# Kernel optimization log

Hardware: AMD Instinct MI355X
Metric: run time of the kernel (lower is better)

Reference implementation:

```python
import jax, jax.numpy as jnp
import numpy as np

B, S, HID = 1, 8192, 768
H, D = 12, 64          # num heads, head dim (HID = H*D)
W = 256                # one-sided attention window


def _shift_chunks(xc, C):
    # xc: [B, C, w, H, D] -> prev/next chunk copies padded with zeros
    prev = jnp.pad(xc, ((0, 0), (1, 0), (0, 0), (0, 0), (0, 0)))[:, :C]
    nxt = jnp.pad(xc, ((0, 0), (0, 1), (0, 0), (0, 0), (0, 0)))[:, 1:]
    return jnp.concatenate([prev, xc, nxt], axis=2)  # [B, C, 3w, H, D]


def sliding_window_attention(q, k, v, w):
    # q,k,v: [B, S, H, D]; q already scaled. Band width 2w+1.
    b, s, h, d = q.shape
    c = s // w
    qc = q.reshape(b, c, w, h, d)
    k3 = _shift_chunks(k.reshape(b, c, w, h, d), c)  # [b,c,3w,h,d]
    v3 = _shift_chunks(v.reshape(b, c, w, h, d), c)
    # scores of each query chunk against its 3-chunk key neighborhood
    scores3 = jnp.einsum('bcxhd,bcyhd->bhcxy', qc, k3)  # [b,h,c,w,3w]
    rows = jnp.arange(w)
    offs = jnp.arange(2 * w + 1)
    gidx = rows[:, None] + offs[None, :]  # [w, 2w+1] local key index p+j
    band = scores3[..., rows[:, None], gidx]  # [b,h,c,w,2w+1]
    # mask keys outside [0, S) (same effect as mask_invalid_locations)
    gq = jnp.arange(s).reshape(c, w)                    # global query pos
    keypos = gq[..., None] + (offs - w)                 # [c,w,2w+1]
    valid = (keypos >= 0) & (keypos < s)
    band = jnp.where(valid[None, None], band, -jnp.inf)
    prob = jax.nn.softmax(band, axis=-1)
    prob = jnp.where(valid[None, None], prob, 0.0)
    # scatter band probs back to 3w layout, then banded PV matmul
    prob3 = jnp.zeros(band.shape[:-1] + (3 * w,), band.dtype)
    prob3 = prob3.at[..., rows[:, None], gidx].set(prob)  # [b,h,c,w,3w]
    ctx = jnp.einsum('bhcxy,bcyhd->bcxhd', prob3, v3)
    return ctx.reshape(b, s, h, d)


def setup_inputs() -> dict:
    key = jax.random.key(0)
    ks = jax.random.split(key, 4)
    sc = 1.0 / np.sqrt(HID)
    return {
        'hidden_states': jax.random.normal(ks[0], (B, S, HID), jnp.float32),
        'Wq': jax.random.normal(ks[1], (HID, HID), jnp.float32) * sc,
        'bq': jnp.zeros((HID,), jnp.float32),
        'Wk': jax.random.normal(ks[2], (HID, HID), jnp.float32) * sc,
        'bk': jnp.zeros((HID,), jnp.float32),
        'Wv': jax.random.normal(ks[3], (HID, HID), jnp.float32) * sc,
        'bv': jnp.zeros((HID,), jnp.float32),
    }


def reference(hidden_states, Wq, bq, Wk, bk, Wv, bv):
    b, s, hid = hidden_states.shape
    q = (hidden_states @ Wq + bq).reshape(b, s, H, D)
    k = (hidden_states @ Wk + bk).reshape(b, s, H, D)
    v = (hidden_states @ Wv + bv).reshape(b, s, H, D)
    q = q / jnp.asarray(np.sqrt(D), q.dtype)
    ctx = sliding_window_attention(q, k, v, W)  # [b,s,H,D]
    return ctx.reshape(b, s, hid)
```

## Files before the change

kernel.cpp:

```cpp
#include <hip/hip_runtime.h>
#include <hip/hip_bf16.h>

#define S_LEN 8192
#define HID 768
#define NH 12
#define HD 64
#define WIN 256

typedef __bf16 bf16x8 __attribute__((ext_vector_type(8)));
typedef float f32x4 __attribute__((ext_vector_type(4)));
using bf16_t = __hip_bfloat16;

#define MFMA(a, b, c) __builtin_amdgcn_mfma_f32_16x16x32_bf16(a, b, c, 0, 0, 0)

__device__ __forceinline__ void gl2lds16(const bf16_t* g, bf16_t* l) {
  __builtin_amdgcn_global_load_lds(
      (const __attribute__((address_space(1))) void*)g,
      (__attribute__((address_space(3))) void*)l, 16, 0, 0);
}

__global__ __launch_bounds__(256) void prep(const float* __restrict__ hs,
                                            bf16_t* __restrict__ hb,
                                            const float* __restrict__ Wq,
                                            const float* __restrict__ Wk,
                                            const float* __restrict__ Wv,
                                            bf16_t* __restrict__ Wt) {
  int bx = blockIdx.x;
  int tid = threadIdx.x;
  if (bx < 6144) {
    int i = (bx * 256 + tid) * 4;
    float4 v = *reinterpret_cast<const float4*>(hs + i);
    union { ushort4 u; bf16_t b[4]; } H;
    H.b[0] = __float2bfloat16(v.x);
    H.b[1] = __float2bfloat16(v.y);
    H.b[2] = __float2bfloat16(v.z);
    H.b[3] = __float2bfloat16(v.w);
    *reinterpret_cast<ushort4*>(hb + i) = H.u;
    return;
  }
  __shared__ float t[32][33];
  int b = bx - 6144;
  int z = b / 576;
  int r = b % 576;
  int n0 = (r / 24) * 32, k0 = (r % 24) * 32;
  const float* src = (z == 0) ? Wq : ((z == 1) ? Wk : Wv);
  int tx = tid & 31, ty = tid >> 5;
  for (int i = 0; i < 4; ++i)
    t[ty + i * 8][tx] = src[(k0 + ty + i * 8) * HID + n0 + tx];
  __syncthreads();
  bf16_t* dst = Wt + z * HID * HID;
  for (int i = 0; i < 4; ++i)
    dst[(n0 + ty + i * 8) * HID + k0 + tx] = __float2bfloat16(t[tx][ty + i * 8]);
}

__global__ __launch_bounds__(256) void qkv_gemm(
    const bf16_t* __restrict__ hb, const bf16_t* __restrict__ Wt,
    const float* __restrict__ bq, const float* __restrict__ bk,
    const float* __restrict__ bv,
    bf16_t* __restrict__ Qw, bf16_t* __restrict__ Kw, bf16_t* __restrict__ Vt) {
  __shared__ __align__(16) bf16_t sA[2][128 * 64];
  __shared__ __align__(16) bf16_t sB[2][128 * 64];
  int m0 = blockIdx.x * 128;
  int zq = blockIdx.y / 6;
  int nn0 = (blockIdx.y % 6) * 128;
  int n0g = zq * HID + nn0;
  int tid = threadIdx.x;
  int w = tid >> 6, lane = tid & 63, lm = lane & 15, qd = lane >> 4;
  int wm = w & 1, wn = w >> 1;

  int srow = w * 8 + (lane >> 3);
  int sc8 = (lane & 7) ^ ((lane >> 3) & 7);
  const bf16_t* gA = hb + (m0 + srow) * HID + sc8 * 8;
  const bf16_t* gB = Wt + (n0g + srow) * HID + sc8 * 8;
  int sx0 = lm & 7;

#define QSTAGE(kk, bb)                                                     \
  {                                                                        \
    _Pragma("unroll") for (int u = 0; u < 4; ++u) {                        \
      gl2lds16(gA + (u * 32) * HID + (kk), sA[bb] + u * 2048 + w * 512);   \
      gl2lds16(gB + (u * 32) * HID + (kk), sB[bb] + u * 2048 + w * 512);   \
    }                                                                      \
  }

  QSTAGE(0, 0);
  __syncthreads();

  f32x4 acc[4][4] = {};
  for (int kt = 0; kt < 12; ++kt) {
    int b = kt & 1;
    if (kt < 11) QSTAGE((kt + 1) * 64, b ^ 1);
#pragma unroll
    for (int half = 0; half < 2; ++half) {
      int ca = (qd + 4 * half) ^ sx0;
      bf16x8 fa[4], fb[4];
#pragma unroll
      for (int i = 0; i < 4; ++i) {
        fa[i] = *reinterpret_cast<const bf16x8*>(
            sA[b] + (wm * 64 + i * 16 + lm) * 64 + ca * 8);
        fb[i] = *reinterpret_cast<const bf16x8*>(
            sB[b] + (wn * 64 + i * 16 + lm) * 64 + ca * 8);
      }
      if (zq == 2) {
#pragma unroll
        for (int i = 0; i < 4; ++i)
#pragma unroll
          for (int j = 0; j < 4; ++j)
            acc[i][j] = MFMA(fb[i], fa[j], acc[i][j]);
      } else {
#pragma unroll
        for (int i = 0; i < 4; ++i)
#pragma unroll
          for (int j = 0; j < 4; ++j)
            acc[i][j] = MFMA(fa[i], fb[j], acc[i][j]);
      }
    }
    __syncthreads();
  }

  if (zq != 2) {
    const float* bias = zq ? bk : bq;
    bf16_t* dst = zq ? Kw : Qw;
    float scale = zq ? 1.0f : 0.125f;
#pragma unroll
    for (int j = 0; j < 4; ++j) {
      int nl = nn0 + wn * 64 + j * 16 + lm;
      float bb = bias[nl];
      int h = nl >> 6, d = nl & 63;
#pragma unroll
      for (int i = 0; i < 4; ++i)
#pragma unroll
        for (int r = 0; r < 4; ++r) {
          int m = m0 + wm * 64 + i * 16 + qd * 4 + r;
          dst[(h * S_LEN + m) * HD + d] =
              __float2bfloat16((acc[i][j][r] + bb) * scale);
        }
    }
  } else {
#pragma unroll
    for (int i = 0; i < 4; ++i)
#pragma unroll
      for (int r = 0; r < 4; ++r) {
        int nl = nn0 + wn * 64 + i * 16 + qd * 4 + r;
        float bb = bv[nl];
#pragma unroll
        for (int j = 0; j < 4; ++j) {
          int m = m0 + wm * 64 + j * 16 + lm;
          Vt[nl * S_LEN + m] = __float2bfloat16(acc[i][j][r] + bb);
        }
      }
  }
}

__global__ __launch_bounds__(256, 4) void swa_kernel(
    const bf16_t* __restrict__ Qw, const bf16_t* __restrict__ Kw,
    const bf16_t* __restrict__ Vt, float* __restrict__ out) {
  __shared__ __align__(16) bf16_t sK[2][64 * 64];
  __shared__ __align__(16) bf16_t sV[2][64 * 64];
  __shared__ __align__(16) bf16_t sP[4 * 16 * 64];
  int h = blockIdx.y;
  int nb = blockIdx.x;
  int q0 = (((nb & 7) << 4) | (nb >> 3)) * 64;
  int tid = threadIdx.x;
  int w = tid >> 6, lane = tid & 63, lm = lane & 15, qd = lane >> 4;
  int xb = q0 + w * 16;

  int qoff = (h * S_LEN + xb + lm) * HD + qd * 8;
  bf16x8 aq0 = *reinterpret_cast<const bf16x8*>(Qw + qoff);
  bf16x8 aq1 = *reinterpret_cast<const bf16x8*>(Qw + qoff + 32);

  f32x4 o[4] = {};
  float lsum = 0.f;

  int y_begin = q0 - WIN; if (y_begin < 0) y_begin = 0;
  int y_end = q0 + 64 + WIN; if (y_end > S_LEN) y_end = S_LEN;
  int ntiles = (y_end - y_begin) >> 6;
  const bf16_t* Kh = Kw + h * S_LEN * HD;
  const bf16_t* Vh = Vt + h * HD * S_LEN;
  bf16_t* sPw = sP + w * 16 * 64;

  int srow = w * 8 + (lane >> 3);
  int sc8 = (lane & 7) ^ ((lane >> 3) & 7);
  int sx0 = lm & 7;

#define STAGE(y0, b)                                                    \
  {                                                                     \
    const bf16_t* kg = Kh + ((y0) + srow) * HD + sc8 * 8;               \
    gl2lds16(kg, &sK[b][w * 512]);                                      \
    gl2lds16(kg + 32 * HD, &sK[b][2048 + w * 512]);                     \
    const bf16_t* vg = Vh + srow * S_LEN + (y0) + sc8 * 8;              \
    gl2lds16(vg, &sV[b][w * 512]);                                      \
    gl2lds16(vg + 32 * S_LEN, &sV[b][2048 + w * 512]);                  \
  }

  STAGE(y_begin, 0);
  __syncthreads();

  for (int t = 0; t < ntiles; ++t) {
    int y0 = y_begin + t * 64;
    if (t + 1 < ntiles) STAGE(y0 + 64, (t + 1) & 1);
    int b = t & 1;
    f32x4 s[4] = {};
#pragma unroll
    for (int nt = 0; nt < 4; ++nt) {
      const bf16_t* kr = &sK[b][(nt * 16 + lm) * 64];
      bf16x8 b0 = *reinterpret_cast<const bf16x8*>(kr + (qd ^ sx0) * 8);
      bf16x8 b1 = *reinterpret_cast<const bf16x8*>(kr + ((qd + 4) ^ sx0) * 8);
      s[nt] = MFMA(b0, aq0, s[nt]);
      s[nt] = MFMA(b1, aq1, s[nt]);
    }
    int dy = y0 - q0;
    bool edge = (dy > 192) || (dy < -192);
#pragma unroll
    for (int nt = 0; nt < 4; ++nt) {
      union { ushort4 u; bf16_t b[4]; } P;
#pragma unroll
      for (int r = 0; r < 4; ++r) {
        float pv;
        if (edge) {
          int dlt = (y0 + nt * 16 + qd * 4 + r) - (xb + lm);
          pv = (dlt <= WIN && dlt >= -WIN) ? __expf(s[nt][r]) : 0.f;
        } else {
          pv = __expf(s[nt][r]);
        }
        lsum += pv;
        P.b[r] = __float2bfloat16(pv);
      }
      *reinterpret_cast<ushort4*>(
          sPw + lm * 64 + (((2 * nt + (qd >> 1)) ^ sx0) * 8) + (qd & 1) * 4) =
          P.u;
    }
    bf16x8 ap0 =
        *reinterpret_cast<const bf16x8*>(sPw + lm * 64 + ((qd ^ sx0) * 8));
    bf16x8 ap1 = *reinterpret_cast<const bf16x8*>(sPw + lm * 64 +
                                                  (((qd + 4) ^ sx0) * 8));
#pragma unroll
    for (int nt = 0; nt < 4; ++nt) {
      const bf16_t* vr = &sV[b][(nt * 16 + lm) * 64];
      bf16x8 v0 = *reinterpret_cast<const bf16x8*>(vr + (qd ^ sx0) * 8);
      bf16x8 v1 = *reinterpret_cast<const bf16x8*>(vr + ((qd + 4) ^ sx0) * 8);
      o[nt] = MFMA(ap0, v0, o[nt]);
      o[nt] = MFMA(ap1, v1, o[nt]);
    }
    __syncthreads();
  }
  lsum += __shfl_xor(lsum, 16);
  lsum += __shfl_xor(lsum, 32);
#pragma unroll
  for (int r = 0; r < 4; ++r) {
    float inv = 1.f / __shfl(lsum, qd * 4 + r);
    int x = xb + qd * 4 + r;
#pragma unroll
    for (int nt = 0; nt < 4; ++nt)
      out[x * HID + h * HD + nt * 16 + lm] = o[nt][r] * inv;
  }
}

extern "C" void kernel_launch(void* const* d_in, const int* in_sizes, int n_in,
                              void* d_out, int out_size, void* d_ws, size_t ws_size,
                              hipStream_t stream) {
  const float* hs = (const float*)d_in[0];
  const float* Wq = (const float*)d_in[1];
  const float* bq = (const float*)d_in[2];
  const float* Wk = (const float*)d_in[3];
  const float* bk = (const float*)d_in[4];
  const float* Wv = (const float*)d_in[5];
  const float* bv = (const float*)d_in[6];
  float* out = (float*)d_out;

  const int NSH = S_LEN * HID;
  const int NW = 3 * HID * HID;
  bf16_t* p = (bf16_t*)d_ws;
  bf16_t* hb = p; p += NSH;
  bf16_t* Wt = p; p += NW;
  bf16_t* Qw = p; p += NSH;
  bf16_t* Kw = p; p += NSH;
  bf16_t* Vt = p; p += NSH;

  prep<<<dim3(6144 + 1728), dim3(256), 0, stream>>>(hs, hb, Wq, Wk, Wv, Wt);
  qkv_gemm<<<dim3(64, 18), dim3(256), 0, stream>>>(
      hb, Wt, bq, bk, bv, Qw, Kw, Vt);
  swa_kernel<<<dim3(128, 12), dim3(256), 0, stream>>>(Qw, Kw, Vt, out);
}
```

Before: 161.3 us.

## Process 128 queries per block so each K/V tile serves two query groups

Each sliding-window attention block now covers 128 query rows instead of 64, with each wave handling two 16-row query groups against the same staged K/V tile. The aim is to amortize K/V global-to-LDS staging and LDS fragment reads over twice the queries, cutting redundant halo loads. In exchange the grid halves to 768 blocks, register and LDS use per block grow (launch bound lowered to 3 blocks), and each block iterates over more key tiles, some of them only partly inside the band for a given wave.

```diff
diff --git a/kernel.cpp b/kernel.cpp
--- a/kernel.cpp
+++ b/kernel.cpp
@@ -151,32 +151,34 @@
   }
 }
 
-__global__ __launch_bounds__(256, 4) void swa_kernel(
+__global__ __launch_bounds__(256, 3) void swa_kernel(
     const bf16_t* __restrict__ Qw, const bf16_t* __restrict__ Kw,
     const bf16_t* __restrict__ Vt, float* __restrict__ out) {
   __shared__ __align__(16) bf16_t sK[2][64 * 64];
   __shared__ __align__(16) bf16_t sV[2][64 * 64];
-  __shared__ __align__(16) bf16_t sP[4 * 16 * 64];
+  __shared__ __align__(16) bf16_t sP[4 * 32 * 64];
   int h = blockIdx.y;
   int nb = blockIdx.x;
-  int q0 = (((nb & 7) << 4) | (nb >> 3)) * 64;
+  int q0 = (((nb & 7) << 3) | (nb >> 3)) * 128;
   int tid = threadIdx.x;
   int w = tid >> 6, lane = tid & 63, lm = lane & 15, qd = lane >> 4;
-  int xb = q0 + w * 16;
+  int xb = q0 + w * 32;
 
   int qoff = (h * S_LEN + xb + lm) * HD + qd * 8;
-  bf16x8 aq0 = *reinterpret_cast<const bf16x8*>(Qw + qoff);
-  bf16x8 aq1 = *reinterpret_cast<const bf16x8*>(Qw + qoff + 32);
-
-  f32x4 o[4] = {};
-  float lsum = 0.f;
+  bf16x8 aq00 = *reinterpret_cast<const bf16x8*>(Qw + qoff);
+  bf16x8 aq01 = *reinterpret_cast<const bf16x8*>(Qw + qoff + 32);
+  bf16x8 aq10 = *reinterpret_cast<const bf16x8*>(Qw + qoff + 16 * HD);
+  bf16x8 aq11 = *reinterpret_cast<const bf16x8*>(Qw + qoff + 16 * HD + 32);
+
+  f32x4 o0[4] = {}, o1[4] = {};
+  float lsum0 = 0.f, lsum1 = 0.f;
 
   int y_begin = q0 - WIN; if (y_begin < 0) y_begin = 0;
-  int y_end = q0 + 64 + WIN; if (y_end > S_LEN) y_end = S_LEN;
+  int y_end = q0 + 128 + WIN; if (y_end > S_LEN) y_end = S_LEN;
   int ntiles = (y_end - y_begin) >> 6;
   const bf16_t* Kh = Kw + h * S_LEN * HD;
   const bf16_t* Vh = Vt + h * HD * S_LEN;
-  bf16_t* sPw = sP + w * 16 * 64;
+  bf16_t* sPw = sP + w * 32 * 64;
 
   int srow = w * 8 + (lane >> 3);
   int sc8 = (lane & 7) ^ ((lane >> 3) & 7);
@@ -199,59 +201,80 @@
     int y0 = y_begin + t * 64;
     if (t + 1 < ntiles) STAGE(y0 + 64, (t + 1) & 1);
     int b = t & 1;
-    f32x4 s[4] = {};
+    f32x4 s0[4] = {}, s1[4] = {};
 #pragma unroll
     for (int nt = 0; nt < 4; ++nt) {
       const bf16_t* kr = &sK[b][(nt * 16 + lm) * 64];
       bf16x8 b0 = *reinterpret_cast<const bf16x8*>(kr + (qd ^ sx0) * 8);
       bf16x8 b1 = *reinterpret_cast<const bf16x8*>(kr + ((qd + 4) ^ sx0) * 8);
-      s[nt] = MFMA(b0, aq0, s[nt]);
-      s[nt] = MFMA(b1, aq1, s[nt]);
-    }
-    int dy = y0 - q0;
-    bool edge = (dy > 192) || (dy < -192);
-#pragma unroll
-    for (int nt = 0; nt < 4; ++nt) {
-      union { ushort4 u; bf16_t b[4]; } P;
-#pragma unroll
-      for (int r = 0; r < 4; ++r) {
-        float pv;
-        if (edge) {
-          int dlt = (y0 + nt * 16 + qd * 4 + r) - (xb + lm);
-          pv = (dlt <= WIN && dlt >= -WIN) ? __expf(s[nt][r]) : 0.f;
-        } else {
-          pv = __expf(s[nt][r]);
+      s0[nt] = MFMA(b0, aq00, s0[nt]);
+      s0[nt] = MFMA(b1, aq01, s0[nt]);
+      s1[nt] = MFMA(b0, aq10, s1[nt]);
+      s1[nt] = MFMA(b1, aq11, s1[nt]);
+    }
+    int dyw = y0 - xb;
+    bool edge = (dyw > 193) || (dyw < -225);
+#pragma unroll
+    for (int g = 0; g < 2; ++g) {
+      const f32x4* sg = g ? s1 : s0;
+      float lacc = 0.f;
+#pragma unroll
+      for (int nt = 0; nt < 4; ++nt) {
+        union { ushort4 u; bf16_t b[4]; } P;
+#pragma unroll
+        for (int r = 0; r < 4; ++r) {
+          float pv;
+          if (edge) {
+            int dlt = (y0 + nt * 16 + qd * 4 + r) - (xb + g * 16 + lm);
+            pv = (dlt <= WIN && dlt >= -WIN) ? __expf(sg[nt][r]) : 0.f;
+          } else {
+            pv = __expf(sg[nt][r]);
+          }
+          lacc += pv;
+          P.b[r] = __float2bfloat16(pv);
         }
-        lsum += pv;
-        P.b[r] = __float2bfloat16(pv);
+        *reinterpret_cast<ushort4*>(
+            sPw + (g * 16 + lm) * 64 +
+            (((2 * nt + (qd >> 1)) ^ sx0) * 8) + (qd & 1) * 4) = P.u;
       }
-      *reinterpret_cast<ushort4*>(
-          sPw + lm * 64 + (((2 * nt + (qd >> 1)) ^ sx0) * 8) + (qd & 1) * 4) =
-          P.u;
-    }
-    bf16x8 ap0 =
+      if (g) lsum1 += lacc; else lsum0 += lacc;
+    }
+    bf16x8 ap00 =
         *reinterpret_cast<const bf16x8*>(sPw + lm * 64 + ((qd ^ sx0) * 8));
-    bf16x8 ap1 = *reinterpret_cast<const bf16x8*>(sPw + lm * 64 +
-                                                  (((qd + 4) ^ sx0) * 8));
+    bf16x8 ap01 = *reinterpret_cast<const bf16x8*>(sPw + lm * 64 +
+                                                   (((qd + 4) ^ sx0) * 8));
+    bf16x8 ap10 = *reinterpret_cast<const bf16x8*>(sPw + (16 + lm) * 64 +
+                                                   ((qd ^ sx0) * 8));
+    bf16x8 ap11 = *reinterpret_cast<const bf16x8*>(sPw + (16 + lm) * 64 +
+                                                   (((qd + 4) ^ sx0) * 8));
 #pragma unroll
     for (int nt = 0; nt < 4; ++nt) {
       const bf16_t* vr = &sV[b][(nt * 16 + lm) * 64];
       bf16x8 v0 = *reinterpret_cast<const bf16x8*>(vr + (qd ^ sx0) * 8);
       bf16x8 v1 = *reinterpret_cast<const bf16x8*>(vr + ((qd + 4) ^ sx0) * 8);
-      o[nt] = MFMA(ap0, v0, o[nt]);
-      o[nt] = MFMA(ap1, v1, o[nt]);
+      o0[nt] = MFMA(ap00, v0, o0[nt]);
+      o0[nt] = MFMA(ap01, v1, o0[nt]);
+      o1[nt] = MFMA(ap10, v0, o1[nt]);
+      o1[nt] = MFMA(ap11, v1, o1[nt]);
     }
     __syncthreads();
   }
-  lsum += __shfl_xor(lsum, 16);
-  lsum += __shfl_xor(lsum, 32);
+  lsum0 += __shfl_xor(lsum0, 16);
+  lsum0 += __shfl_xor(lsum0, 32);
+  lsum1 += __shfl_xor(lsum1, 16);
+  lsum1 += __shfl_xor(lsum1, 32);
 #pragma unroll
   for (int r = 0; r < 4; ++r) {
-    float inv = 1.f / __shfl(lsum, qd * 4 + r);
-    int x = xb + qd * 4 + r;
+    float inv0 = 1.f / __shfl(lsum0, qd * 4 + r);
+    int x0 = xb + qd * 4 + r;
 #pragma unroll
     for (int nt = 0; nt < 4; ++nt)
-      out[x * HID + h * HD + nt * 16 + lm] = o[nt][r] * inv;
+      out[x0 * HID + h * HD + nt * 16 + lm] = o0[nt][r] * inv0;
+    float inv1 = 1.f / __shfl(lsum1, qd * 4 + r);
+    int x1 = xb + 16 + qd * 4 + r;
+#pragma unroll
+    for (int nt = 0; nt < 4; ++nt)
+      out[x1 * HID + h * HD + nt * 16 + lm] = o1[nt][r] * inv1;
   }
 }
 
@@ -279,5 +302,5 @@
   prep<<<dim3(6144 + 1728), dim3(256), 0, stream>>>(hs, hb, Wq, Wk, Wv, Wt);
   qkv_gemm<<<dim3(64, 18), dim3(256), 0, stream>>>(
       hb, Wt, bq, bk, bv, Qw, Kw, Vt);
-  swa_kernel<<<dim3(128, 12), dim3(256), 0, stream>>>(Qw, Kw, Vt, out);
-}
+  swa_kernel<<<dim3(64, 12), dim3(256), 0, stream>>>(Qw, Kw, Vt, out);
+}
```

After: 160.1 us. Within noise of the previous version (-0.7%).
